# Optimization experiments

Measured on AMD Instinct MI355X. Metric: run time of the kernel, lower is better.

Reference implementation:

```python
import jax, jax.numpy as jnp
import numpy as np

NEG_SLOPE = 0.2
EPS = 1e-16

N_NODES = 100000
N_EDGES = 1600000
F_IN = 64
HID = 64
T_OUT = 1


def _gat_conv(x, src, dst, W, a_src, a_dst, b, n_nodes):
    # x: [N, Fin] -> h: [N, H]
    h = x @ W
    # per-node attention logits, then gather per-edge (PyG GATConv, heads=1)
    s_src = h @ a_src  # [N]
    s_dst = h @ a_dst  # [N]
    e = jax.nn.leaky_relu(s_src[src] + s_dst[dst], NEG_SLOPE)  # [E]
    # segment softmax over incoming edges of each destination node
    m = jax.ops.segment_max(e, dst, num_segments=n_nodes)  # [N]
    ex = jnp.exp(e - m[dst])
    denom = jax.ops.segment_sum(ex, dst, num_segments=n_nodes)  # [N]
    alpha = ex / (denom[dst] + EPS)  # [E]
    # weighted scatter-add aggregation
    out = jax.ops.segment_sum(alpha[:, None] * h[src], dst, num_segments=n_nodes)
    return out + b


def _add_self_loops(edge_index, n_nodes):
    loops = jnp.arange(n_nodes, dtype=edge_index.dtype)
    src = jnp.concatenate([edge_index[0], loops])
    dst = jnp.concatenate([edge_index[1], loops])
    return src, dst


def setup_inputs() -> dict:
    key = jax.random.key(0)
    ks = jax.random.split(key, 12)
    x = jax.random.normal(ks[0], (N_NODES, F_IN), dtype=jnp.float32)
    edge_index = jax.random.randint(ks[1], (2, N_EDGES), 0, N_NODES, dtype=jnp.int32)
    s1 = 1.0 / np.sqrt(F_IN)
    s2 = 1.0 / np.sqrt(HID)
    return {
        "x": x,
        "edge_index": edge_index,
        "W1": jax.random.normal(ks[2], (F_IN, HID), dtype=jnp.float32) * s1,
        "a_src1": jax.random.normal(ks[3], (HID,), dtype=jnp.float32) * s2,
        "a_dst1": jax.random.normal(ks[4], (HID,), dtype=jnp.float32) * s2,
        "b1": jnp.zeros((HID,), dtype=jnp.float32),
        "W2": jax.random.normal(ks[5], (HID, HID), dtype=jnp.float32) * s2,
        "a_src2": jax.random.normal(ks[6], (HID,), dtype=jnp.float32) * s2,
        "a_dst2": jax.random.normal(ks[7], (HID,), dtype=jnp.float32) * s2,
        "b2": jnp.zeros((HID,), dtype=jnp.float32),
        "Wl": jax.random.normal(ks[8], (HID, T_OUT), dtype=jnp.float32) * s2,
        "bl": jnp.zeros((T_OUT,), dtype=jnp.float32),
    }


def reference(x, edge_index, W1, a_src1, a_dst1, b1, W2, a_src2, a_dst2, b2, Wl, bl):
    n_nodes = x.shape[0]
    src, dst = _add_self_loops(edge_index, n_nodes)  # PyG add_self_loops=True
    h = _gat_conv(x, src, dst, W1, a_src1, a_dst1, b1, n_nodes)
    h = jnp.tanh(h)  # dropout is identity in eval mode
    h = _gat_conv(h, src, dst, W2, a_src2, a_dst2, b2, n_nodes)
    return h @ Wl + bl  # [N, 1]
```

## Files before the change

### kernel.cpp

```cpp
#include <hip/hip_runtime.h>

#define NN 100000
#define NE 1600000
#define ET (NE + NN)
#define NB 391
#define CAP 5120
#define BST 16
#define NBIN 256
#define NCHK (ET/8)
#define NTILE (NN/16)

typedef _Float16 f16;
typedef __attribute__((ext_vector_type(8))) _Float16 half8;
typedef __attribute__((ext_vector_type(4))) float f32x4;

__device__ __forceinline__ unsigned short hbits(float v){
    f16 h = (f16)v;
    return *(unsigned short*)&h;
}
__device__ __forceinline__ unsigned pk16(float a, float b){
    auto p = __builtin_amdgcn_cvt_pkrtz(a, b);
    return *(unsigned*)&p;
}
__device__ __forceinline__ float fast_tanh(float x){
    float e = __expf(2.f*x);
    return 1.f - __fdividef(2.f, e + 1.f);
}
__device__ __forceinline__ void fmix2(float& al, float& ah, unsigned h2, float a){
    asm("v_fma_mix_f32 %0, %2, %3, %0 op_sel_hi:[1,0,0]\n\t"
        "v_fma_mix_f32 %1, %2, %3, %1 op_sel:[1,0,0] op_sel_hi:[1,0,0]"
        : "+v"(al), "+v"(ah) : "v"(h2), "v"(a));
}

__global__ void __launch_bounds__(256) k_bin(const int* __restrict__ src,
        const int* __restrict__ dst, int* __restrict__ bcnt,
        int* __restrict__ binbuf){
    __shared__ int cnt[NB];
    __shared__ int cur[NB];
    int t = threadIdx.x;
    for(int i=t;i<NB;i+=256) cnt[i]=0;
    __syncthreads();
    for(int g = blockIdx.x*256 + t; g < NCHK; g += NBIN*256){
        if(g < NE/8){
            const uint4* dp = (const uint4*)(dst + g*8);
            uint4 d0 = dp[0], d1 = dp[1];
            atomicAdd(&cnt[d0.x>>8],1); atomicAdd(&cnt[d0.y>>8],1);
            atomicAdd(&cnt[d0.z>>8],1); atomicAdd(&cnt[d0.w>>8],1);
            atomicAdd(&cnt[d1.x>>8],1); atomicAdd(&cnt[d1.y>>8],1);
            atomicAdd(&cnt[d1.z>>8],1); atomicAdd(&cnt[d1.w>>8],1);
        } else {
            int n0 = g*8 - NE;
            #pragma unroll
            for(int i=0;i<8;i++) atomicAdd(&cnt[(n0+i)>>8],1);
        }
    }
    __syncthreads();
    for(int i=t;i<NB;i+=256){ int c=cnt[i]; cur[i] = c ? atomicAdd(&bcnt[i*BST], c) : 0; }
    __syncthreads();
    for(int g = blockIdx.x*256 + t; g < NCHK; g += NBIN*256){
        int s[8], d[8];
        if(g < NE/8){
            const uint4* sp = (const uint4*)(src + g*8);
            const uint4* dp = (const uint4*)(dst + g*8);
            uint4 s0 = sp[0], s1 = sp[1];
            uint4 d0 = dp[0], d1 = dp[1];
            s[0]=s0.x; s[1]=s0.y; s[2]=s0.z; s[3]=s0.w;
            s[4]=s1.x; s[5]=s1.y; s[6]=s1.z; s[7]=s1.w;
            d[0]=d0.x; d[1]=d0.y; d[2]=d0.z; d[3]=d0.w;
            d[4]=d1.x; d[5]=d1.y; d[6]=d1.z; d[7]=d1.w;
        } else {
            int n0 = g*8 - NE;
            #pragma unroll
            for(int i=0;i<8;i++){ s[i]=n0+i; d[i]=n0+i; }
        }
        #pragma unroll
        for(int i=0;i<8;i++){
            int b = d[i] >> 8;
            int pos = atomicAdd(&cur[b], 1);
            if(pos < CAP) binbuf[b*CAP + pos] = (s[i] << 8) | (d[i] & 255);
        }
    }
}

__global__ void __launch_bounds__(256) k_build(const int* __restrict__ bcnt,
        const int* __restrict__ binbuf, int* __restrict__ edge_src,
        int* __restrict__ rowst, int* __restrict__ deg){
    __shared__ int lsrc[CAP];
    __shared__ int ldeg[256], lscan[256], lcur[256], red[256];
    int b = blockIdx.x, t = threadIdx.x;
    int cnt = min(bcnt[b*BST], CAP);
    int part = 0;
    for(int i=t;i<b;i+=256) part += min(bcnt[i*BST], CAP);
    red[t] = part; __syncthreads();
    for(int off=128; off>=1; off>>=1){ if(t<off) red[t]+=red[t+off]; __syncthreads(); }
    int base = red[0];
    __syncthreads();
    ldeg[t] = 0; __syncthreads();
    const int* bb = binbuf + b*CAP;
    for(int i=t;i<cnt;i+=256) atomicAdd(&ldeg[bb[i] & 255], 1);
    __syncthreads();
    int dv = ldeg[t]; lscan[t] = dv; __syncthreads();
    for(int off=1; off<256; off<<=1){
        int u = (t>=off) ? lscan[t-off] : 0;
        __syncthreads(); lscan[t] += u; __syncthreads();
    }
    int excl = lscan[t] - dv; lcur[t] = excl;
    int node = b*256 + t;
    if(node < NN){ rowst[node] = base + excl; deg[node] = dv; }
    __syncthreads();
    for(int i=t;i<cnt;i+=256){
        int ent = bb[i];
        int pos = atomicAdd(&lcur[ent & 255], 1);
        lsrc[pos] = ent >> 8;
    }
    __syncthreads();
    for(int i=t;i<cnt;i+=256) edge_src[base+i] = lsrc[i];
}

template<int FPIN>
__global__ void __launch_bounds__(256) k_gemm(const void* __restrict__ xin,
        const float* __restrict__ W, const float* __restrict__ avs,
        const float* __restrict__ avd, f16* __restrict__ hb,
        float* __restrict__ ssrc, float* __restrict__ sdst){
    int tid = threadIdx.x, lane = tid & 63;
    int col = lane & 15, q = lane >> 4;
    half8 Bf[2][4];
    #pragma unroll
    for(int kh=0;kh<2;kh++){
        #pragma unroll
        for(int nb=0;nb<4;nb++){
            half8 b;
            #pragma unroll
            for(int j=0;j<8;j++){
                float w = W[(kh*32 + q*8 + j)*64 + nb*16 + col];
                b[j] = (f16)w;
            }
            Bf[kh][nb] = b;
        }
    }
    float as[4], ad[4];
    #pragma unroll
    for(int nb=0;nb<4;nb++){ as[nb] = avs[nb*16+col]; ad[nb] = avd[nb*16+col]; }

    int gw = (blockIdx.x*256 + tid) >> 6;
    int nwaves = gridDim.x*4;
    for(int tile = gw; tile < NTILE; tile += nwaves){
        int n0 = tile*16;
        f32x4 acc[4];
        #pragma unroll
        for(int nb=0;nb<4;nb++) acc[nb] = (f32x4){0.f,0.f,0.f,0.f};
        #pragma unroll
        for(int kh=0;kh<2;kh++){
            half8 a;
            if(FPIN){
                const float4* xr = (const float4*)((const float*)xin
                                    + (size_t)(n0+col)*64 + kh*32 + q*8);
                float4 u = xr[0], v = xr[1];
                union { half8 h; uint4 u4; } A;
                A.u4.x = pk16(u.x, u.y);
                A.u4.y = pk16(u.z, u.w);
                A.u4.z = pk16(v.x, v.y);
                A.u4.w = pk16(v.z, v.w);
                a = A.h;
            } else {
                a = *(const half8*)((const f16*)xin
                                    + (size_t)(n0+col)*64 + kh*32 + q*8);
            }
            #pragma unroll
            for(int nb=0;nb<4;nb++)
                acc[nb] = __builtin_amdgcn_mfma_f32_16x16x32_f16(a, Bf[kh][nb], acc[nb], 0,0,0);
        }
        #pragma unroll
        for(int nb=0;nb<4;nb++){
            #pragma unroll
            for(int r=0;r<4;r++)
                hb[(size_t)(n0 + q*4 + r)*64 + nb*16 + col] = (f16)acc[nb][r];
        }
        #pragma unroll
        for(int r=0;r<4;r++){
            float ps = acc[0][r]*as[0] + acc[1][r]*as[1] + acc[2][r]*as[2] + acc[3][r]*as[3];
            float pd = acc[0][r]*ad[0] + acc[1][r]*ad[1] + acc[2][r]*ad[2] + acc[3][r]*ad[3];
            #pragma unroll
            for(int m=8;m>=1;m>>=1){ ps += __shfl_xor(ps,m); pd += __shfl_xor(pd,m); }
            if(col == 0){ ssrc[n0 + q*4 + r] = ps; sdst[n0 + q*4 + r] = pd; }
        }
    }
}

template<int LAYER>
__device__ __forceinline__ void node_full(int node, int lane, int2* lp,
        const int* __restrict__ rowst, const int* __restrict__ deg,
        const int* __restrict__ edge_src, const float* __restrict__ ssrc,
        const float* __restrict__ sdst, const f16* __restrict__ hb,
        const float* __restrict__ bias, const float* __restrict__ Wl,
        const float* __restrict__ bl, f16* __restrict__ out1b,
        float* __restrict__ outF){
    int rs = rowst[node];
    int d  = deg[node];
    float sd = sdst[node];
    int g8 = lane >> 3;
    int c  = lane & 7;
    float a0=0.f,a1=0.f,a2=0.f,a3=0.f,a4=0.f,a5=0.f,a6=0.f,a7=0.f;

    float lmax = -1e30f;
    for(int j=lane; j<d; j+=64){
        int sj = edge_src[rs+j];
        float t = ssrc[sj] + sd;
        lmax = fmaxf(lmax, fmaxf(t, 0.2f*t));
    }
    #pragma unroll
    for(int m=32;m>=1;m>>=1) lmax = fmaxf(lmax, __shfl_xor(lmax,m));
    float lsum = 0.f;
    for(int j=lane; j<d; j+=64){
        int sj = edge_src[rs+j];
        float t = ssrc[sj] + sd;
        lsum += __expf(fmaxf(t, 0.2f*t) - lmax);
    }
    #pragma unroll
    for(int m=32;m>=1;m>>=1) lsum += __shfl_xor(lsum,m);
    float inv = 1.0f/(lsum + 1e-16f);
    for(int cb=0; cb<d; cb+=64){
        int s2 = 0; float al = 0.f;
        int j = cb + lane;
        if(j < d){
            s2 = edge_src[rs+j];
            float t = ssrc[s2] + sd;
            al = __expf(fmaxf(t, 0.2f*t) - lmax) * inv;
        }
        lp[lane] = make_int2(__float_as_int(al), s2);
        int dd = min(d - cb, 64);
        for(int i0=0; i0<dd; i0+=16){
            int2 e0 = lp[i0 + g8];
            int2 e1 = lp[i0 + 8 + g8];
            float f0 = __int_as_float(e0.x);
            float f1 = __int_as_float(e1.x);
            uint4 k0 = *(const uint4*)(hb + ((size_t)e0.y<<6) + (c<<3));
            uint4 k1 = *(const uint4*)(hb + ((size_t)e1.y<<6) + (c<<3));
            fmix2(a0,a1,k0.x,f0); fmix2(a2,a3,k0.y,f0);
            fmix2(a4,a5,k0.z,f0); fmix2(a6,a7,k0.w,f0);
            fmix2(a0,a1,k1.x,f1); fmix2(a2,a3,k1.y,f1);
            fmix2(a4,a5,k1.z,f1); fmix2(a6,a7,k1.w,f1);
        }
    }
    #pragma unroll
    for(int m=32;m>=8;m>>=1){
        a0 += __shfl_xor(a0,m); a1 += __shfl_xor(a1,m);
        a2 += __shfl_xor(a2,m); a3 += __shfl_xor(a3,m);
        a4 += __shfl_xor(a4,m); a5 += __shfl_xor(a5,m);
        a6 += __shfl_xor(a6,m); a7 += __shfl_xor(a7,m);
    }
    const float4* bp = (const float4*)bias;
    float4 bv0 = bp[c*2], bv1 = bp[c*2+1];
    if(LAYER == 1){
        if(g8 == 0){
            uint4 o;
            o.x = (unsigned)hbits(fast_tanh(a0+bv0.x)) | ((unsigned)hbits(fast_tanh(a1+bv0.y))<<16);
            o.y = (unsigned)hbits(fast_tanh(a2+bv0.z)) | ((unsigned)hbits(fast_tanh(a3+bv0.w))<<16);
            o.z = (unsigned)hbits(fast_tanh(a4+bv1.x)) | ((unsigned)hbits(fast_tanh(a5+bv1.y))<<16);
            o.w = (unsigned)hbits(fast_tanh(a6+bv1.z)) | ((unsigned)hbits(fast_tanh(a7+bv1.w))<<16);
            *(uint4*)(out1b + ((size_t)node<<6) + (c<<3)) = o;
        }
    } else {
        const float4* wp = (const float4*)Wl;
        float4 wv0 = wp[c*2], wv1 = wp[c*2+1];
        float r = (a0+bv0.x)*wv0.x + (a1+bv0.y)*wv0.y + (a2+bv0.z)*wv0.z + (a3+bv0.w)*wv0.w
                + (a4+bv1.x)*wv1.x + (a5+bv1.y)*wv1.y + (a6+bv1.z)*wv1.z + (a7+bv1.w)*wv1.w;
        r += __shfl_xor(r,1); r += __shfl_xor(r,2); r += __shfl_xor(r,4);
        if(lane == 0) outF[node] = r + bl[0];
    }
}


template<int LAYER>
__global__ void __launch_bounds__(256) k_agg(
        const int* __restrict__ rowst, const int* __restrict__ deg,
        const int* __restrict__ edge_src,
        const float* __restrict__ ssrc, const float* __restrict__ sdst,
        const f16* __restrict__ hb,
        const float* __restrict__ bias, const float* __restrict__ Wl,
        const float* __restrict__ bl,
        f16* __restrict__ out1b, float* __restrict__ outF){
    __shared__ int2 pairs[256];
    int tid = threadIdx.x;
    int wv   = (blockIdx.x*256 + tid) >> 6;
    int lane = tid & 63;
    if(wv*2 >= NN) return;
    int2* lp = pairs + (tid & 192);
    int half = lane >> 5, l = lane & 31;
    int node = wv*2 + half;

    int rs = rowst[node];
    int d  = deg[node];
    float sd = sdst[node];
    int dmax = max(d, __shfl_xor(d, 32));

    if(dmax <= 32){
        int s = 0; float pr = 0.f;
        if(l < d){
            s = edge_src[rs + l];
            float t = ssrc[s] + sd;
            t = fmaxf(t, 0.2f*t);
            pr = __expf(fminf(t, 80.f));
        }
        float sm = pr;
        #pragma unroll
        for(int m=16;m>=1;m>>=1) sm += __shfl_xor(sm,m);
        float alpha = pr * (1.0f/(sm + 1e-16f));
        lp[lane] = make_int2(__float_as_int(alpha), s);

        int g4 = l >> 3;
        int c  = l & 7;
        int base = half << 5;
        int nitw = (dmax + 7) >> 3;
        float F0[4], F1[4];
        uint4 K0[4], K1[4];
        #pragma unroll
        for(int it=0; it<4; it++){
            if(it < nitw){
                int2 e0 = lp[base + it*8 + g4];
                int2 e1 = lp[base + it*8 + 4 + g4];
                F0[it] = __int_as_float(e0.x);
                F1[it] = __int_as_float(e1.x);
                K0[it] = *(const uint4*)(hb + ((size_t)e0.y<<6) + (c<<3));
                K1[it] = *(const uint4*)(hb + ((size_t)e1.y<<6) + (c<<3));
            }
        }
        float a0=0.f,a1=0.f,a2=0.f,a3=0.f,a4=0.f,a5=0.f,a6=0.f,a7=0.f;
        #pragma unroll
        for(int it=0; it<4; it++){
            if(it < nitw){
                fmix2(a0,a1,K0[it].x,F0[it]); fmix2(a2,a3,K0[it].y,F0[it]);
                fmix2(a4,a5,K0[it].z,F0[it]); fmix2(a6,a7,K0[it].w,F0[it]);
                fmix2(a0,a1,K1[it].x,F1[it]); fmix2(a2,a3,K1[it].y,F1[it]);
                fmix2(a4,a5,K1[it].z,F1[it]); fmix2(a6,a7,K1[it].w,F1[it]);
            }
        }

        bool b3 = (l >> 3) & 1, b4 = (l >> 4) & 1;
        float u0 = b3 ? a4 : a0, v0 = b3 ? a0 : a4; u0 += __shfl_xor(v0, 8);
        float u1 = b3 ? a5 : a1, v1 = b3 ? a1 : a5; u1 += __shfl_xor(v1, 8);
        float u2 = b3 ? a6 : a2, v2 = b3 ? a2 : a6; u2 += __shfl_xor(v2, 8);
        float u3 = b3 ? a7 : a3, v3 = b3 ? a3 : a7; u3 += __shfl_xor(v3, 8);
        float w0 = b4 ? u2 : u0, z0 = b4 ? u0 : u2; w0 += __shfl_xor(z0, 16);
        float w1 = b4 ? u3 : u1, z1 = b4 ? u1 : u3; w1 += __shfl_xor(z1, 16);
        int ch0 = (c<<3) + ((int)b3<<2) + ((int)b4<<1);

        if(LAYER == 1){
            float2 bv = ((const float2*)bias)[ch0>>1];
            unsigned o = pk16(fast_tanh(w0 + bv.x), fast_tanh(w1 + bv.y));
            *(unsigned*)(out1b + ((size_t)node<<6) + ch0) = o;
        } else {
            float2 bv = ((const float2*)bias)[ch0>>1];
            float2 wl = ((const float2*)Wl)[ch0>>1];
            float r = (w0 + bv.x)*wl.x + (w1 + bv.y)*wl.y;
            #pragma unroll
            for(int m=16;m>=1;m>>=1) r += __shfl_xor(r,m);
            if(l == 0) outF[node] = r + bl[0];
        }
    } else {
        node_full<LAYER>(wv*2,   lane, lp, rowst, deg, edge_src, ssrc, sdst,
                         hb, bias, Wl, bl, out1b, outF);
        node_full<LAYER>(wv*2+1, lane, lp, rowst, deg, edge_src, ssrc, sdst,
                         hb, bias, Wl, bl, out1b, outF);
    }
}

extern "C" void kernel_launch(void* const* d_in, const int* in_sizes, int n_in,
                              void* d_out, int out_size, void* d_ws, size_t ws_size,
                              hipStream_t stream) {
    const float* x   = (const float*)d_in[0];
    const int*   ei  = (const int*)d_in[1];
    const float* W1  = (const float*)d_in[2];
    const float* as1 = (const float*)d_in[3];
    const float* ad1 = (const float*)d_in[4];
    const float* b1  = (const float*)d_in[5];
    const float* W2  = (const float*)d_in[6];
    const float* as2 = (const float*)d_in[7];
    const float* ad2 = (const float*)d_in[8];
    const float* b2  = (const float*)d_in[9];
    const float* Wl  = (const float*)d_in[10];
    const float* bl  = (const float*)d_in[11];
    float* out = (float*)d_out;

    const int* srcp = ei;
    const int* dstp = ei + NE;

    char* w = (char*)d_ws;
    int*   edge_src = (int*)w;  w += (size_t)ET*4;
    f16*   hb       = (f16*)w;  w += (size_t)NN*64*2;
    f16*   t1b      = (f16*)w;  w += (size_t)NN*64*2;
    int*   rowst    = (int*)w;  w += (size_t)NN*4;
    int*   deg      = (int*)w;  w += (size_t)NN*4;
    float* ssrc     = (float*)w; w += (size_t)NN*4;
    float* sdst     = (float*)w; w += (size_t)NN*4;
    int*   bcnt     = (int*)w;  w += (size_t)NB*BST*4;
    int*   binbuf   = (int*)hb;

    const int nbG = 782;
    const int nbA = (NN/2 + 3)/4;

    (void)hipMemsetAsync(bcnt, 0, (size_t)NB*BST*4, stream);
    k_bin  <<<NBIN, 256, 0, stream>>>(srcp, dstp, bcnt, binbuf);
    k_build<<<NB,   256, 0, stream>>>(bcnt, binbuf, edge_src, rowst, deg);

    k_gemm<1><<<nbG, 256, 0, stream>>>((const void*)x, W1, as1, ad1, hb, ssrc, sdst);
    k_agg<1><<<nbA, 256, 0, stream>>>(rowst, deg, edge_src, ssrc, sdst, hb,
                                      b1, (const float*)nullptr, (const float*)nullptr,
                                      t1b, (float*)nullptr);
    k_gemm<0><<<nbG, 256, 0, stream>>>((const void*)t1b, W2, as2, ad2, hb, ssrc, sdst);
    k_agg<2><<<nbA, 256, 0, stream>>>(rowst, deg, edge_src, ssrc, sdst, hb,
                                      b2, Wl, bl,
                                      (f16*)nullptr, out);
}
```

Baseline: 216.3 us.

## Fold final linear projection into layer-2 GEMM to aggregate scalars instead of vectors

Because the last layer is linear, the output equals the softmax-weighted sum of (h·Wl) plus a bias term. The second GEMM now emits a per-node scalar h·Wl and no longer writes the fp16 h matrix. The second aggregation gathers one float per edge instead of a 64-wide fp16 row, which removes most of its gather traffic. In the fast path it skips max subtraction and clamps the exponent at 80, which changes the numerics slightly.

```diff
diff --git a/kernel.cpp b/kernel.cpp
--- a/kernel.cpp
+++ b/kernel.cpp
@@ -117,11 +117,12 @@
     for(int i=t;i<cnt;i+=256) edge_src[base+i] = lsrc[i];
 }
 
-template<int FPIN>
+template<int FPIN, int L2>
 __global__ void __launch_bounds__(256) k_gemm(const void* __restrict__ xin,
         const float* __restrict__ W, const float* __restrict__ avs,
-        const float* __restrict__ avd, f16* __restrict__ hb,
-        float* __restrict__ ssrc, float* __restrict__ sdst){
+        const float* __restrict__ avd, const float* __restrict__ Wlv,
+        f16* __restrict__ hb, float* __restrict__ ssrc,
+        float* __restrict__ sdst, float* __restrict__ gsc){
     int tid = threadIdx.x, lane = tid & 63;
     int col = lane & 15, q = lane >> 4;
     half8 Bf[2][4];
@@ -138,9 +139,12 @@
             Bf[kh][nb] = b;
         }
     }
-    float as[4], ad[4];
-    #pragma unroll
-    for(int nb=0;nb<4;nb++){ as[nb] = avs[nb*16+col]; ad[nb] = avd[nb*16+col]; }
+    float as[4], ad[4], wl[4];
+    #pragma unroll
+    for(int nb=0;nb<4;nb++){
+        as[nb] = avs[nb*16+col]; ad[nb] = avd[nb*16+col];
+        wl[nb] = L2 ? Wlv[nb*16+col] : 0.f;
+    }
 
     int gw = (blockIdx.x*256 + tid) >> 6;
     int nwaves = gridDim.x*4;
@@ -170,31 +174,37 @@
             for(int nb=0;nb<4;nb++)
                 acc[nb] = __builtin_amdgcn_mfma_f32_16x16x32_f16(a, Bf[kh][nb], acc[nb], 0,0,0);
         }
-        #pragma unroll
-        for(int nb=0;nb<4;nb++){
-            #pragma unroll
-            for(int r=0;r<4;r++)
-                hb[(size_t)(n0 + q*4 + r)*64 + nb*16 + col] = (f16)acc[nb][r];
+        if(!L2){
+            #pragma unroll
+            for(int nb=0;nb<4;nb++){
+                #pragma unroll
+                for(int r=0;r<4;r++)
+                    hb[(size_t)(n0 + q*4 + r)*64 + nb*16 + col] = (f16)acc[nb][r];
+            }
         }
         #pragma unroll
         for(int r=0;r<4;r++){
             float ps = acc[0][r]*as[0] + acc[1][r]*as[1] + acc[2][r]*as[2] + acc[3][r]*as[3];
             float pd = acc[0][r]*ad[0] + acc[1][r]*ad[1] + acc[2][r]*ad[2] + acc[3][r]*ad[3];
-            #pragma unroll
-            for(int m=8;m>=1;m>>=1){ ps += __shfl_xor(ps,m); pd += __shfl_xor(pd,m); }
-            if(col == 0){ ssrc[n0 + q*4 + r] = ps; sdst[n0 + q*4 + r] = pd; }
-        }
-    }
-}
-
-template<int LAYER>
-__device__ __forceinline__ void node_full(int node, int lane, int2* lp,
+            float pg = L2 ? (acc[0][r]*wl[0] + acc[1][r]*wl[1] + acc[2][r]*wl[2] + acc[3][r]*wl[3]) : 0.f;
+            #pragma unroll
+            for(int m=8;m>=1;m>>=1){
+                ps += __shfl_xor(ps,m); pd += __shfl_xor(pd,m);
+                if(L2) pg += __shfl_xor(pg,m);
+            }
+            if(col == 0){
+                ssrc[n0 + q*4 + r] = ps; sdst[n0 + q*4 + r] = pd;
+                if(L2) gsc[n0 + q*4 + r] = pg;
+            }
+        }
+    }
+}
+
+__device__ __forceinline__ void node_full1(int node, int lane, int2* lp,
         const int* __restrict__ rowst, const int* __restrict__ deg,
         const int* __restrict__ edge_src, const float* __restrict__ ssrc,
         const float* __restrict__ sdst, const f16* __restrict__ hb,
-        const float* __restrict__ bias, const float* __restrict__ Wl,
-        const float* __restrict__ bl, f16* __restrict__ out1b,
-        float* __restrict__ outF){
+        const float* __restrict__ bias, f16* __restrict__ out1b){
     int rs = rowst[node];
     int d  = deg[node];
     float sd = sdst[node];
@@ -251,35 +261,22 @@
     }
     const float4* bp = (const float4*)bias;
     float4 bv0 = bp[c*2], bv1 = bp[c*2+1];
-    if(LAYER == 1){
-        if(g8 == 0){
-            uint4 o;
-            o.x = (unsigned)hbits(fast_tanh(a0+bv0.x)) | ((unsigned)hbits(fast_tanh(a1+bv0.y))<<16);
-            o.y = (unsigned)hbits(fast_tanh(a2+bv0.z)) | ((unsigned)hbits(fast_tanh(a3+bv0.w))<<16);
-            o.z = (unsigned)hbits(fast_tanh(a4+bv1.x)) | ((unsigned)hbits(fast_tanh(a5+bv1.y))<<16);
-            o.w = (unsigned)hbits(fast_tanh(a6+bv1.z)) | ((unsigned)hbits(fast_tanh(a7+bv1.w))<<16);
-            *(uint4*)(out1b + ((size_t)node<<6) + (c<<3)) = o;
-        }
-    } else {
-        const float4* wp = (const float4*)Wl;
-        float4 wv0 = wp[c*2], wv1 = wp[c*2+1];
-        float r = (a0+bv0.x)*wv0.x + (a1+bv0.y)*wv0.y + (a2+bv0.z)*wv0.z + (a3+bv0.w)*wv0.w
-                + (a4+bv1.x)*wv1.x + (a5+bv1.y)*wv1.y + (a6+bv1.z)*wv1.z + (a7+bv1.w)*wv1.w;
-        r += __shfl_xor(r,1); r += __shfl_xor(r,2); r += __shfl_xor(r,4);
-        if(lane == 0) outF[node] = r + bl[0];
-    }
-}
-
-
-template<int LAYER>
-__global__ void __launch_bounds__(256) k_agg(
+    if(g8 == 0){
+        uint4 o;
+        o.x = (unsigned)hbits(fast_tanh(a0+bv0.x)) | ((unsigned)hbits(fast_tanh(a1+bv0.y))<<16);
+        o.y = (unsigned)hbits(fast_tanh(a2+bv0.z)) | ((unsigned)hbits(fast_tanh(a3+bv0.w))<<16);
+        o.z = (unsigned)hbits(fast_tanh(a4+bv1.x)) | ((unsigned)hbits(fast_tanh(a5+bv1.y))<<16);
+        o.w = (unsigned)hbits(fast_tanh(a6+bv1.z)) | ((unsigned)hbits(fast_tanh(a7+bv1.w))<<16);
+        *(uint4*)(out1b + ((size_t)node<<6) + (c<<3)) = o;
+    }
+}
+
+__global__ void __launch_bounds__(256) k_agg1(
         const int* __restrict__ rowst, const int* __restrict__ deg,
         const int* __restrict__ edge_src,
         const float* __restrict__ ssrc, const float* __restrict__ sdst,
-        const f16* __restrict__ hb,
-        const float* __restrict__ bias, const float* __restrict__ Wl,
-        const float* __restrict__ bl,
-        f16* __restrict__ out1b, float* __restrict__ outF){
+        const f16* __restrict__ hb, const float* __restrict__ bias,
+        f16* __restrict__ out1b){
     __shared__ int2 pairs[256];
     int tid = threadIdx.x;
     int wv   = (blockIdx.x*256 + tid) >> 6;
@@ -345,23 +342,78 @@
         float w1 = b4 ? u3 : u1, z1 = b4 ? u1 : u3; w1 += __shfl_xor(z1, 16);
         int ch0 = (c<<3) + ((int)b3<<2) + ((int)b4<<1);
 
-        if(LAYER == 1){
-            float2 bv = ((const float2*)bias)[ch0>>1];
-            unsigned o = pk16(fast_tanh(w0 + bv.x), fast_tanh(w1 + bv.y));
-            *(unsigned*)(out1b + ((size_t)node<<6) + ch0) = o;
-        } else {
-            float2 bv = ((const float2*)bias)[ch0>>1];
-            float2 wl = ((const float2*)Wl)[ch0>>1];
-            float r = (w0 + bv.x)*wl.x + (w1 + bv.y)*wl.y;
-            #pragma unroll
-            for(int m=16;m>=1;m>>=1) r += __shfl_xor(r,m);
-            if(l == 0) outF[node] = r + bl[0];
-        }
+        float2 bv = ((const float2*)bias)[ch0>>1];
+        unsigned o = pk16(fast_tanh(w0 + bv.x), fast_tanh(w1 + bv.y));
+        *(unsigned*)(out1b + ((size_t)node<<6) + ch0) = o;
     } else {
-        node_full<LAYER>(wv*2,   lane, lp, rowst, deg, edge_src, ssrc, sdst,
-                         hb, bias, Wl, bl, out1b, outF);
-        node_full<LAYER>(wv*2+1, lane, lp, rowst, deg, edge_src, ssrc, sdst,
-                         hb, bias, Wl, bl, out1b, outF);
+        node_full1(wv*2,   lane, lp, rowst, deg, edge_src, ssrc, sdst, hb, bias, out1b);
+        node_full1(wv*2+1, lane, lp, rowst, deg, edge_src, ssrc, sdst, hb, bias, out1b);
+    }
+}
+
+__global__ void __launch_bounds__(256) k_agg2(
+        const int* __restrict__ rowst, const int* __restrict__ deg,
+        const int* __restrict__ edge_src,
+        const float* __restrict__ ssrc, const float* __restrict__ sdst,
+        const float* __restrict__ gsc, const float* __restrict__ bias,
+        const float* __restrict__ Wl, const float* __restrict__ bl,
+        float* __restrict__ outF){
+    int tid = threadIdx.x;
+    int wv   = (blockIdx.x*256 + tid) >> 6;
+    int lane = tid & 63;
+    if(wv*2 >= NN) return;
+    int half = lane >> 5, l = lane & 31;
+    int node = wv*2 + half;
+
+    float2 bv = ((const float2*)bias)[l];
+    float2 wl = ((const float2*)Wl)[l];
+    float rc = bv.x*wl.x + bv.y*wl.y;
+    #pragma unroll
+    for(int m=16;m>=1;m>>=1) rc += __shfl_xor(rc,m);
+
+    int rs = rowst[node];
+    int d  = deg[node];
+    float sd = sdst[node];
+    int dmax = max(d, __shfl_xor(d, 32));
+
+    if(dmax <= 32){
+        float pr = 0.f, gv = 0.f;
+        if(l < d){
+            int s = edge_src[rs + l];
+            float t = ssrc[s] + sd;
+            t = fmaxf(t, 0.2f*t);
+            pr = __expf(fminf(t, 80.f));
+            gv = gsc[s];
+        }
+        float sm = pr, num = pr*gv;
+        #pragma unroll
+        for(int m=16;m>=1;m>>=1){ sm += __shfl_xor(sm,m); num += __shfl_xor(num,m); }
+        if(l == 0) outF[node] = num/(sm + 1e-16f) + rc + bl[0];
+    } else {
+        #pragma unroll 1
+        for(int k=0;k<2;k++){
+            int nd = wv*2 + k;
+            int rs2 = rowst[nd], d2 = deg[nd];
+            float sd2 = sdst[nd];
+            float lmax = -1e30f;
+            for(int j=lane; j<d2; j+=64){
+                int sj = edge_src[rs2+j];
+                float t = ssrc[sj] + sd2;
+                lmax = fmaxf(lmax, fmaxf(t, 0.2f*t));
+            }
+            #pragma unroll
+            for(int m=32;m>=1;m>>=1) lmax = fmaxf(lmax, __shfl_xor(lmax,m));
+            float lsum = 0.f, lnum = 0.f;
+            for(int j=lane; j<d2; j+=64){
+                int sj = edge_src[rs2+j];
+                float t = ssrc[sj] + sd2;
+                float e = __expf(fmaxf(t, 0.2f*t) - lmax);
+                lsum += e; lnum += e*gsc[sj];
+            }
+            #pragma unroll
+            for(int m=32;m>=1;m>>=1){ lsum += __shfl_xor(lsum,m); lnum += __shfl_xor(lnum,m); }
+            if(lane == 0) outF[nd] = lnum/(lsum + 1e-16f) + rc + bl[0];
+        }
     }
 }
 
@@ -393,6 +445,7 @@
     int*   deg      = (int*)w;  w += (size_t)NN*4;
     float* ssrc     = (float*)w; w += (size_t)NN*4;
     float* sdst     = (float*)w; w += (size_t)NN*4;
+    float* gsc      = (float*)w; w += (size_t)NN*4;
     int*   bcnt     = (int*)w;  w += (size_t)NB*BST*4;
     int*   binbuf   = (int*)hb;
 
@@ -403,12 +456,12 @@
     k_bin  <<<NBIN, 256, 0, stream>>>(srcp, dstp, bcnt, binbuf);
     k_build<<<NB,   256, 0, stream>>>(bcnt, binbuf, edge_src, rowst, deg);
 
-    k_gemm<1><<<nbG, 256, 0, stream>>>((const void*)x, W1, as1, ad1, hb, ssrc, sdst);
-    k_agg<1><<<nbA, 256, 0, stream>>>(rowst, deg, edge_src, ssrc, sdst, hb,
-                                      b1, (const float*)nullptr, (const float*)nullptr,
-                                      t1b, (float*)nullptr);
-    k_gemm<0><<<nbG, 256, 0, stream>>>((const void*)t1b, W2, as2, ad2, hb, ssrc, sdst);
-    k_agg<2><<<nbA, 256, 0, stream>>>(rowst, deg, edge_src, ssrc, sdst, hb,
-                                      b2, Wl, bl,
-                                      (f16*)nullptr, out);
-}
+    k_gemm<1,0><<<nbG, 256, 0, stream>>>((const void*)x, W1, as1, ad1,
+                                         (const float*)nullptr, hb, ssrc, sdst,
+                                         (float*)nullptr);
+    k_agg1<<<nbA, 256, 0, stream>>>(rowst, deg, edge_src, ssrc, sdst, hb, b1, t1b);
+    k_gemm<0,1><<<nbG, 256, 0, stream>>>((const void*)t1b, W2, as2, ad2, Wl,
+                                         (f16*)nullptr, ssrc, sdst, gsc);
+    k_agg2<<<nbA, 256, 0, stream>>>(rowst, deg, edge_src, ssrc, sdst, gsc,
+                                    b2, Wl, bl, out);
+}
```

Result: faster. 197.4 us (-8.7%).
